# Optimization experiments

Measured on AMD Instinct MI355X. Metric: run time of the kernel, lower is better.

The kernel has to match this reference:

```python
import jax, jax.numpy as jnp
import numpy as np
from jax import lax

RATIOS = (0.5, 1.0, 2.0)
LEVEL_SCALES = (4, 8, 16, 32)
FEAT_STRIDE = (4, 8, 16, 32)
BASE_SIZE = 16.0
NMS_THRESH = 0.7
PRE_NMS = 2000
POST_NMS = 300
MIN_SIZE = 16.0
SCALE = 1.0


def _anchor_base(scale):
    # chainercv-style anchor base: (y1, x1, y2, x2) centered at base_size/2
    py = px = BASE_SIZE / 2.0
    ab = np.zeros((len(RATIOS), 4), np.float32)
    for i, r in enumerate(RATIOS):
        h = BASE_SIZE * scale * np.sqrt(r)
        w = BASE_SIZE * scale * np.sqrt(1.0 / r)
        ab[i] = [py - h / 2.0, px - w / 2.0, py + h / 2.0, px + w / 2.0]
    return ab


def _shifted_anchors(level, hh, ww):
    ab = _anchor_base(LEVEL_SCALES[level])
    stride = FEAT_STRIDE[level]
    sy = np.arange(0, hh * stride, stride)
    sx = np.arange(0, ww * stride, stride)
    sx, sy = np.meshgrid(sx, sy)
    shift = np.stack((sy.ravel(), sx.ravel(), sy.ravel(), sx.ravel()), axis=1)
    A, K = ab.shape[0], shift.shape[0]
    anchor = ab.reshape(1, A, 4) + shift.reshape(1, K, 4).transpose(1, 0, 2)
    return anchor.reshape(K * A, 4).astype(np.float32)


def _conv(x, w, b, pad):
    y = lax.conv_general_dilated(x, w, (1, 1), [(pad, pad), (pad, pad)],
                                 dimension_numbers=("NCHW", "OIHW", "NCHW"))
    return y + b[None, :, None, None]


def _iou_matrix(b):
    y1, x1, y2, x2 = b[:, 0], b[:, 1], b[:, 2], b[:, 3]
    area = (y2 - y1) * (x2 - x1)
    iy = jnp.maximum(0.0, jnp.minimum(y2[:, None], y2[None, :]) - jnp.maximum(y1[:, None], y1[None, :]))
    ix = jnp.maximum(0.0, jnp.minimum(x2[:, None], x2[None, :]) - jnp.maximum(x1[:, None], x1[None, :]))
    inter = iy * ix
    return inter / (area[:, None] + area[None, :] - inter + 1e-10)


def _greedy_nms(boxes, keep0):
    # boxes are sorted by descending score; sequential greedy suppression
    n = boxes.shape[0]
    iou = _iou_matrix(boxes)  # [PRE_NMS, PRE_NMS]
    idx = jnp.arange(n)

    def body(i, keep):
        sup = jnp.where(keep[i], iou[i] > NMS_THRESH, False) & (idx > i)
        return keep & ~sup

    return lax.fori_loop(0, n, body, keep0)


def _proposal_single(loc, fg, anchors, img_h, img_w):
    # loc2bbox decode
    ah = anchors[:, 2] - anchors[:, 0]
    aw = anchors[:, 3] - anchors[:, 1]
    acy = anchors[:, 0] + 0.5 * ah
    acx = anchors[:, 1] + 0.5 * aw
    cy = loc[:, 0] * ah + acy
    cx = loc[:, 1] * aw + acx
    h = jnp.exp(loc[:, 2]) * ah
    w = jnp.exp(loc[:, 3]) * aw
    boxes = jnp.stack([cy - 0.5 * h, cx - 0.5 * w, cy + 0.5 * h, cx + 0.5 * w], axis=-1)
    hi = jnp.array([img_h, img_w, img_h, img_w], dtype=boxes.dtype)
    boxes = jnp.clip(boxes, 0.0, hi)
    hs = boxes[:, 2] - boxes[:, 0]
    ws = boxes[:, 3] - boxes[:, 1]
    valid = (hs >= MIN_SIZE * SCALE) & (ws >= MIN_SIZE * SCALE)
    sc = jnp.where(valid, fg, -jnp.inf)
    top_sc, top_idx = lax.top_k(sc, PRE_NMS)
    tb = boxes[top_idx]
    keep = _greedy_nms(tb, top_sc > -jnp.inf)
    order = jnp.argsort(jnp.where(keep, 0, 1), stable=True)[:POST_NMS]
    roi = jnp.where(keep[order][:, None], tb[order], 0.0)
    return roi  # [POST_NMS, 4] zero-padded


def _head(fm, conv1_w, conv1_b, score_w, score_b, loc_w, loc_b):
    B, _, hh, ww = fm.shape
    h = jax.nn.relu(_conv(fm, conv1_w, conv1_b, 1))
    locs = _conv(h, loc_w, loc_b, 0).transpose(0, 2, 3, 1).reshape(B, -1, 4)
    scores = _conv(h, score_w, score_b, 0).transpose(0, 2, 3, 1)  # [B,hh,ww,6]
    fg = jax.nn.softmax(scores.reshape(B, hh, ww, 3, 2), axis=-1)[..., 1].reshape(B, -1)
    return locs, scores.reshape(B, -1, 2), fg


def setup_inputs() -> dict:
    key = jax.random.key(0)
    ks = jax.random.split(key, 10)
    d = {
        "fm0": jax.random.normal(ks[0], (2, 512, 200, 200), jnp.float32),
        "fm1": jax.random.normal(ks[1], (2, 512, 100, 100), jnp.float32),
        "fm2": jax.random.normal(ks[2], (2, 512, 50, 50), jnp.float32),
        "fm3": jax.random.normal(ks[3], (2, 512, 25, 25), jnp.float32),
        "conv1_w": jax.random.normal(ks[4], (512, 512, 3, 3), jnp.float32) * 0.01,
        "conv1_b": jnp.zeros((512,), jnp.float32),
        "score_w": jax.random.normal(ks[5], (6, 512, 1, 1), jnp.float32) * 0.01,
        "score_b": jnp.zeros((6,), jnp.float32),
        "loc_w": jax.random.normal(ks[6], (12, 512, 1, 1), jnp.float32) * 0.01,
        "loc_b": jnp.zeros((12,), jnp.float32),
        "img_h": 800,
        "img_w": 800,
    }
    return d


def reference(fm0, fm1, fm2, fm3, conv1_w, conv1_b, score_w, score_b, loc_w, loc_b, img_h, img_w):
    fms = [fm0, fm1, fm2, fm3]
    B = fm0.shape[0]
    all_locs, all_scores, all_fg, anchors_np = [], [], [], []
    for i, fm in enumerate(fms):
        hh, ww = fm.shape[2], fm.shape[3]
        anchors_np.append(_shifted_anchors(i, hh, ww))
        locs, scores, fg = _head(fm, conv1_w, conv1_b, score_w, score_b, loc_w, loc_b)
        all_locs.append(locs)
        all_scores.append(scores)
        all_fg.append(fg)
    rpn_locs = jnp.concatenate(all_locs, axis=1)      # [B, A, 4]
    rpn_scores = jnp.concatenate(all_scores, axis=1)  # [B, A, 2]
    rpn_fg = jnp.concatenate(all_fg, axis=1)          # [B, A]
    anchors = jnp.asarray(np.concatenate(anchors_np, axis=0))
    # proposal layer operates on detached numpy data in the original
    rois = jax.vmap(lambda l, s: _proposal_single(l, s, anchors, img_h, img_w))(
        lax.stop_gradient(rpn_locs), lax.stop_gradient(rpn_fg))
    rois = rois.reshape(-1, 4)
    roi_indices = jnp.repeat(jnp.arange(B, dtype=jnp.int32), POST_NMS)
    return rpn_locs, rpn_scores, rois, roi_indices, anchors
```

## Files before the change

### kernel.cpp

```cpp
#include <hip/hip_runtime.h>
#include <math.h>

#define NA 159375
static constexpr size_t OFF_LOCS   = 0;
static constexpr size_t OFF_SCORES = 1275000;
static constexpr size_t OFF_ROIS   = 1912500;
static constexpr size_t OFF_RI     = 1914900;
static constexpr size_t OFF_ANCH   = 1915500;
#define MONO_NEGINF 0x007FFFFFu

__global__ void k_wT(const float* __restrict__ w, float* __restrict__ wT) {
  int idx = blockIdx.x * 256 + threadIdx.x;
  if (idx >= 512 * 512 * 9) return;
  int oc = idx & 511;
  int row = idx >> 9;
  int ic = row / 9, tap = row - ic * 9;
  wT[idx] = w[((size_t)oc * 512 + ic) * 9 + tap];
}

__global__
__attribute__((amdgpu_flat_work_group_size(512, 512), amdgpu_waves_per_eu(2, 4)))
void k_conv(
    const float* __restrict__ fm0, const float* __restrict__ fm1,
    const float* __restrict__ fm2, const float* __restrict__ fm3,
    const float* __restrict__ wT,
    const float* __restrict__ cb, const float* __restrict__ locw,
    const float* __restrict__ locb, const float* __restrict__ scow,
    const float* __restrict__ scob, float* __restrict__ out) {
  const int tb_ = blockIdx.x;
  const int b = blockIdx.y;
  int H, locbase, nt, tile;
  const float* fmb;
  if (tb_ < 625)      { H = 200; locbase = 0;     nt = 25; tile = tb_;       fmb = fm0; }
  else if (tb_ < 794) { H = 100; locbase = 40000; nt = 13; tile = tb_ - 625; fmb = fm1; }
  else if (tb_ < 843) { H = 50;  locbase = 50000; nt = 7;  tile = tb_ - 794; fmb = fm2; }
  else                { H = 25;  locbase = 52500; nt = 4;  tile = tb_ - 843; fmb = fm3; }
  const int W = H;
  const int ty_t = tile / nt, tx_t = tile - ty_t * nt;
  const int x0 = tx_t * 8, y0 = ty_t * 8;
  fmb += (size_t)b * 512 * H * W;

  const int tid = threadIdx.x;
  const int pxg = tid & 15, ocg = tid >> 4;
  const int ty = pxg >> 1, tx0 = (pxg & 1) * 4;

  __shared__ alignas(16) union LDS {
    struct { float w[2 * 9 * 512]; float in[2][10][12]; } m;
    struct { float h[64 * 132]; float w1[18 * 128]; } e;
  } lds;

  float acc[4][16];
#pragma unroll
  for (int q = 0; q < 4; q++)
#pragma unroll
    for (int i = 0; i < 16; i++) acc[q][i] = 0.f;

#pragma unroll 1
  for (int ic0 = 0; ic0 < 512; ic0 += 2) {
    __syncthreads();
    const float2* wsrc = reinterpret_cast<const float2*>(wT + (size_t)ic0 * 9 * 512);
    float2* wdst = reinterpret_cast<float2*>(lds.m.w);
#pragma unroll
    for (int r = 0; r < 9; r++) wdst[r * 512 + tid] = wsrc[r * 512 + tid];
    if (tid < 200) {
      int ic = tid / 100, rem = tid % 100, rr = rem / 10, cc = rem % 10;
      int yy = y0 - 1 + rr, xx = x0 - 1 + cc;
      float v = 0.f;
      if (yy >= 0 && yy < H && xx >= 0 && xx < W)
        v = fmb[((size_t)(ic0 + ic) * H + yy) * W + xx];
      lds.m.in[ic][rr][cc] = v;
    }
    __syncthreads();
#pragma unroll
    for (int ic = 0; ic < 2; ic++) {
#pragma unroll
      for (int ky = 0; ky < 3; ky++) {
        const float* rowp = &lds.m.in[ic][ty + ky][tx0];
        float4 rlo = *reinterpret_cast<const float4*>(rowp);
        float2 rhi = *reinterpret_cast<const float2*>(rowp + 4);
        float r[6] = {rlo.x, rlo.y, rlo.z, rlo.w, rhi.x, rhi.y};
#pragma unroll
        for (int kx = 0; kx < 3; kx++) {
          const float4* wp = reinterpret_cast<const float4*>(
              &lds.m.w[(ic * 9 + ky * 3 + kx) * 512 + ocg * 16]);
#pragma unroll
          for (int v4 = 0; v4 < 4; v4++) {
            float4 wv = wp[v4];
#pragma unroll
            for (int q = 0; q < 4; q++) {
              float iv = r[q + kx];
              acc[q][v4 * 4 + 0] = fmaf(iv, wv.x, acc[q][v4 * 4 + 0]);
              acc[q][v4 * 4 + 1] = fmaf(iv, wv.y, acc[q][v4 * 4 + 1]);
              acc[q][v4 * 4 + 2] = fmaf(iv, wv.z, acc[q][v4 * 4 + 2]);
              acc[q][v4 * 4 + 3] = fmaf(iv, wv.w, acc[q][v4 * 4 + 3]);
            }
          }
        }
      }
    }
  }
#pragma unroll
  for (int i = 0; i < 16; i++) {
    float bb = cb[ocg * 16 + i];
#pragma unroll
    for (int q = 0; q < 4; q++) acc[q][i] = fmaxf(__fadd_rn(acc[q][i], bb), 0.f);
  }

  float part[3] = {0.f, 0.f, 0.f};
#pragma unroll 1
  for (int c = 0; c < 4; c++) {
    __syncthreads();
    for (int idx = tid; idx < 18 * 128; idx += 512) {
      int ch = idx >> 7, j = idx & 127;
      lds.e.w1[idx] = (ch < 12) ? locw[ch * 512 + c * 128 + j]
                                : scow[(ch - 12) * 512 + c * 128 + j];
    }
    if ((ocg >> 3) == c) {
      int ocl = (ocg & 7) * 16;
#pragma unroll
      for (int q = 0; q < 4; q++)
#pragma unroll
        for (int i = 0; i < 16; i++)
          lds.e.h[(pxg * 4 + q) * 132 + ocl + i] = acc[q][i];
    }
    __syncthreads();
#pragma unroll
    for (int pp = 0; pp < 3; pp++) {
      int pair = tid + pp * 512;
      if (pair < 1152) {
        int px = pair & 63, ch = pair >> 6;
        const float4* hp = reinterpret_cast<const float4*>(&lds.e.h[px * 132]);
        const float4* wp = reinterpret_cast<const float4*>(&lds.e.w1[ch * 128]);
        float s = part[pp];
#pragma unroll
        for (int j = 0; j < 32; j++) {
          float4 h4 = hp[j], w4 = wp[j];
          s = fmaf(h4.x, w4.x, fmaf(h4.y, w4.y, fmaf(h4.z, w4.z, fmaf(h4.w, w4.w, s))));
        }
        part[pp] = s;
      }
    }
  }
#pragma unroll
  for (int pp = 0; pp < 3; pp++) {
    int pair = tid + pp * 512;
    if (pair < 1152) {
      int px = pair & 63, ch = pair >> 6;
      int y = y0 + (px >> 3), x = x0 + (px & 7);
      if (y < H && x < W) {
        int k = locbase + y * W + x;
        if (ch < 12) {
          int a = ch >> 2, d = ch & 3;
          int n = 3 * k + a;
          out[OFF_LOCS + ((size_t)b * NA + n) * 4 + d] = __fadd_rn(part[pp], locb[ch]);
        } else {
          int s = ch - 12, a = s >> 1, si = s & 1;
          int n = 3 * k + a;
          out[OFF_SCORES + ((size_t)b * NA + n) * 2 + si] = __fadd_rn(part[pp], scob[s]);
        }
      }
    }
  }
}

__global__ void k_anchors(float* __restrict__ out) {
  int n = blockIdx.x * 256 + threadIdx.x;
  if (n >= NA) return;
  int a = n % 3, k = n / 3;
  int base, Wl, stride, scale;
  if (k < 40000)      { base = 0;     Wl = 200; stride = 4;  scale = 4; }
  else if (k < 50000) { base = 40000; Wl = 100; stride = 8;  scale = 8; }
  else if (k < 52500) { base = 50000; Wl = 50;  stride = 16; scale = 16; }
  else                { base = 52500; Wl = 25;  stride = 32; scale = 32; }
  int kk = k - base;
  int ky = kk / Wl, kx = kk - ky * Wl;
  double r = (a == 0) ? 0.5 : ((a == 1) ? 1.0 : 2.0);
  double sc = (double)scale;
  double h = (16.0 * sc) * sqrt(r);
  double w = (16.0 * sc) * sqrt(1.0 / r);
  float ab0 = (float)(8.0 - h / 2.0), ab1 = (float)(8.0 - w / 2.0);
  float ab2 = (float)(8.0 + h / 2.0), ab3 = (float)(8.0 + w / 2.0);
  double sy = (double)(ky * stride), sx = (double)(kx * stride);
  out[OFF_ANCH + (size_t)n * 4 + 0] = (float)((double)ab0 + sy);
  out[OFF_ANCH + (size_t)n * 4 + 1] = (float)((double)ab1 + sx);
  out[OFF_ANCH + (size_t)n * 4 + 2] = (float)((double)ab2 + sy);
  out[OFF_ANCH + (size_t)n * 4 + 3] = (float)((double)ab3 + sx);
}

__global__ void k_zero(unsigned* hhi, unsigned* hlo, unsigned* misc) {
  int i = blockIdx.x * 256 + threadIdx.x;
  if (i < 2 * 65536) { hhi[i] = 0u; hlo[i] = 0u; }
  if (i < 64) misc[i] = 0u;
}

__global__ void k_decode(const float* __restrict__ out, float* __restrict__ boxes,
                         unsigned* __restrict__ keys, const int* __restrict__ ihp,
                         const int* __restrict__ iwp) {
  int n = blockIdx.x * 256 + threadIdx.x;
  int b = blockIdx.y;
  if (n >= NA) return;
  const float* an = out + OFF_ANCH + (size_t)n * 4;
  float a0 = an[0], a1 = an[1], a2 = an[2], a3 = an[3];
  const float* lc = out + OFF_LOCS + ((size_t)b * NA + n) * 4;
  float l0 = lc[0], l1 = lc[1], l2 = lc[2], l3 = lc[3];
  const float* sp = out + OFF_SCORES + ((size_t)b * NA + n) * 2;
  float s0 = sp[0], s1 = sp[1];
  float m = fmaxf(s0, s1);
  float e0 = expf(__fsub_rn(s0, m)), e1 = expf(__fsub_rn(s1, m));
  float fg = __fdiv_rn(e1, __fadd_rn(e0, e1));
  float ah = __fsub_rn(a2, a0), aw = __fsub_rn(a3, a1);
  float acy = __fadd_rn(a0, __fmul_rn(0.5f, ah));
  float acx = __fadd_rn(a1, __fmul_rn(0.5f, aw));
  float cy = __fadd_rn(__fmul_rn(l0, ah), acy);
  float cx = __fadd_rn(__fmul_rn(l1, aw), acx);
  float hh = __fmul_rn(expf(l2), ah), ww = __fmul_rn(expf(l3), aw);
  float y1 = __fsub_rn(cy, __fmul_rn(0.5f, hh));
  float x1 = __fsub_rn(cx, __fmul_rn(0.5f, ww));
  float y2 = __fadd_rn(cy, __fmul_rn(0.5f, hh));
  float x2 = __fadd_rn(cx, __fmul_rn(0.5f, ww));
  float fh = (float)ihp[0], fw = (float)iwp[0];
  y1 = fminf(fmaxf(y1, 0.f), fh); x1 = fminf(fmaxf(x1, 0.f), fw);
  y2 = fminf(fmaxf(y2, 0.f), fh); x2 = fminf(fmaxf(x2, 0.f), fw);
  float hs = __fsub_rn(y2, y1), wsz = __fsub_rn(x2, x1);
  bool valid = (hs >= 16.f) && (wsz >= 16.f);
  float scv = valid ? fg : -INFINITY;
  size_t bi = (size_t)b * NA + n;
  boxes[bi * 4 + 0] = y1; boxes[bi * 4 + 1] = x1;
  boxes[bi * 4 + 2] = y2; boxes[bi * 4 + 3] = x2;
  unsigned u = __float_as_uint(scv);
  keys[bi] = (u & 0x80000000u) ? ~u : (u | 0x80000000u);
}

__global__ void k_hist_hi(const unsigned* __restrict__ keys, unsigned* __restrict__ hhi) {
  int n = blockIdx.x * 256 + threadIdx.x;
  int b = blockIdx.y;
  if (n >= NA) return;
  unsigned k = keys[(size_t)b * NA + n];
  atomicAdd(&hhi[b * 65536 + (k >> 16)], 1u);
}

__global__ void k_hist_lo(const unsigned* __restrict__ keys, const unsigned* __restrict__ misc,
                          unsigned* __restrict__ hlo) {
  int n = blockIdx.x * 256 + threadIdx.x;
  int b = blockIdx.y;
  if (n >= NA) return;
  unsigned bhi = misc[b * 32 + 2];
  unsigned k = keys[(size_t)b * NA + n];
  if ((k >> 16) == bhi) atomicAdd(&hlo[b * 65536 + (k & 0xFFFFu)], 1u);
}

__global__ __launch_bounds__(1024) void k_scan(const unsigned* __restrict__ hist,
                                               unsigned* __restrict__ misc, int mode) {
  int b = blockIdx.x;
  const unsigned* h = hist + (size_t)b * 65536;
  unsigned* mc = misc + b * 32;
  __shared__ unsigned part[1024];
  int t = threadIdx.x;
  unsigned target = (mode == 0) ? 2000u : mc[3];
  unsigned s = 0;
  for (int i = 0; i < 64; i++) s += h[t * 64 + i];
  part[t] = s;
  __syncthreads();
  if (t == 0) {
    unsigned cum = 0; int seg = 0;
    for (int u = 1023; u >= 0; --u) {
      if (cum + part[u] >= target) { seg = u; break; }
      cum += part[u];
    }
    unsigned c2 = cum; int bin = seg * 64;
    for (int v = seg * 64 + 63; v >= seg * 64; --v) {
      if (c2 + h[v] >= target) { bin = v; break; }
      c2 += h[v];
    }
    if (mode == 0) { mc[2] = (unsigned)bin; mc[3] = target - c2; }
    else {
      unsigned T = (mc[2] << 16) | (unsigned)bin;
      unsigned cnt_gt = (2000u - mc[3]) + c2;
      mc[4] = T; mc[5] = cnt_gt; mc[6] = 2000u - cnt_gt;
    }
  }
}

__global__ void k_collect(const unsigned* __restrict__ keys, unsigned* __restrict__ misc,
                          unsigned long long* __restrict__ sel, unsigned* __restrict__ ties) {
  int n = blockIdx.x * 256 + threadIdx.x;
  int b = blockIdx.y;
  if (n >= NA) return;
  unsigned T = misc[b * 32 + 4];
  unsigned k = keys[(size_t)b * NA + n];
  if (k > T) {
    unsigned p = atomicAdd(&misc[b * 32 + 0], 1u);
    if (p < 2048) sel[(size_t)b * 2048 + p] = ((unsigned long long)k << 32) | (unsigned)(~n);
  } else if (k == T) {
    unsigned p = atomicAdd(&misc[b * 32 + 1], 1u);
    if (p < 8192) ties[(size_t)b * 8192 + p] = (unsigned)n;
  }
}

__global__ __launch_bounds__(1024) void k_final(
    const unsigned long long* __restrict__ sel, const unsigned* __restrict__ ties,
    const unsigned* __restrict__ misc, const float* __restrict__ boxes,
    float* __restrict__ tb, unsigned long long* __restrict__ keepw) {
  int b = blockIdx.x, t = threadIdx.x;
  __shared__ unsigned tie_s[8192];
  __shared__ unsigned long long arr[2048];
  __shared__ unsigned long long kw[32];
  unsigned cnt_gt = misc[b * 32 + 5];
  unsigned cnt_eq = misc[b * 32 + 1]; if (cnt_eq > 8192u) cnt_eq = 8192u;
  unsigned T = misc[b * 32 + 4];
  unsigned msort = 64;
  while (msort < cnt_eq) msort <<= 1;
  for (int i = t; i < 8192; i += 1024)
    tie_s[i] = (i < (int)cnt_eq) ? ties[(size_t)b * 8192 + i] : 0xFFFFFFFFu;
  __syncthreads();
  for (unsigned kk = 2; kk <= msort; kk <<= 1)
    for (unsigned j = kk >> 1; j > 0; j >>= 1) {
      for (int i = t; i < (int)msort; i += 1024) {
        int l = i ^ (int)j;
        if (l > i) {
          unsigned a = tie_s[i], c = tie_s[l];
          bool up = ((i & kk) == 0);
          if ((a > c) == up) { tie_s[i] = c; tie_s[l] = a; }
        }
      }
      __syncthreads();
    }
  for (int i = t; i < 2048; i += 1024) {
    unsigned long long v = 0ull;
    if (i < (int)cnt_gt) v = sel[(size_t)b * 2048 + i];
    else if (i < 2000) {
      unsigned n = tie_s[i - cnt_gt];
      v = ((unsigned long long)T << 32) | (unsigned)(~n);
    }
    arr[i] = v;
  }
  __syncthreads();
  for (unsigned kk = 2; kk <= 2048; kk <<= 1)
    for (unsigned j = kk >> 1; j > 0; j >>= 1) {
      for (int i = t; i < 2048; i += 1024) {
        int l = i ^ (int)j;
        if (l > i) {
          unsigned long long a = arr[i], c = arr[l];
          bool dir = ((i & kk) != 0);
          if ((a > c) == dir) { arr[i] = c; arr[l] = a; }
        }
      }
      __syncthreads();
    }
  if (t < 32) kw[t] = 0ull;
  __syncthreads();
  for (int j = t; j < 2000; j += 1024) {
    unsigned long long v = arr[j];
    unsigned n = ~(unsigned)(v & 0xFFFFFFFFull);
    unsigned key = (unsigned)(v >> 32);
    const float* bp = boxes + ((size_t)b * NA + n) * 4;
    float* tp = tb + ((size_t)b * 2000 + j) * 4;
    tp[0] = bp[0]; tp[1] = bp[1]; tp[2] = bp[2]; tp[3] = bp[3];
    if (key > MONO_NEGINF) atomicOr(&kw[j >> 6], 1ull << (j & 63));
  }
  __syncthreads();
  if (t < 32) keepw[b * 32 + t] = kw[t];
}

__device__ __forceinline__ int swz(int i) { return i + (i >> 8); }
__global__ __launch_bounds__(256) void k_iou(const float* __restrict__ tb,
                                             unsigned long long* __restrict__ mask) {
  int b = blockIdx.y;
  __shared__ float bx[8032];
  const float* tbb = tb + (size_t)b * 2000 * 4;
  for (int i = threadIdx.x; i < 8000; i += 256) bx[swz(i)] = tbb[i];
  __syncthreads();
  int il = threadIdx.x >> 5, w = threadIdx.x & 31;
  int i = blockIdx.x * 8 + il;
  int ib = i * 4, ip = ib + (ib >> 8);
  float y1 = bx[ip], x1 = bx[ip + 1], y2 = bx[ip + 2], x2 = bx[ip + 3];
  float ai = __fmul_rn(__fsub_rn(y2, y1), __fsub_rn(x2, x1));
  unsigned long long m = 0ull;
  int j0 = w * 64;
  for (int l = 0; l < 64; l++) {
    int j = j0 + l;
    if (j < 2000 && j > i) {
      int jb = j * 4, jp = jb + (jb >> 8);
      float yy1 = bx[jp], xx1 = bx[jp + 1], yy2 = bx[jp + 2], xx2 = bx[jp + 3];
      float aj = __fmul_rn(__fsub_rn(yy2, yy1), __fsub_rn(xx2, xx1));
      float iy = fmaxf(0.f, __fsub_rn(fminf(y2, yy2), fmaxf(y1, yy1)));
      float ix = fmaxf(0.f, __fsub_rn(fminf(x2, xx2), fmaxf(x1, xx1)));
      float inter = __fmul_rn(iy, ix);
      float den = __fadd_rn(__fsub_rn(__fadd_rn(ai, aj), inter), 1e-10f);
      if (__fdiv_rn(inter, den) > 0.7f) m |= (1ull << l);
    }
  }
  mask[((size_t)b * 2000 + i) * 32 + w] = m;
}

__device__ __forceinline__ unsigned long long shfl64(unsigned long long v, int src) {
  int lo = __shfl((int)(v & 0xFFFFFFFFull), src, 64);
  int hi = __shfl((int)(v >> 32), src, 64);
  return ((unsigned long long)(unsigned)hi << 32) | (unsigned)lo;
}
__global__ __launch_bounds__(64) void k_nms(const unsigned long long* __restrict__ mask,
                                            unsigned long long* __restrict__ keepw) {
  int b = blockIdx.x, lane = threadIdx.x;
  __shared__ unsigned long long rows[64][33];
  unsigned long long k = (lane < 32) ? keepw[b * 32 + lane] : 0ull;
  const unsigned long long* mb = mask + (size_t)b * 2000 * 32;
  for (int c = 0; c < 32; c++) {
    __syncthreads();
    for (int it = 0; it < 32; it++) {
      int idx = it * 64 + lane;
      int r = idx >> 5, w = idx & 31;
      int gi = c * 64 + r;
      rows[r][w] = (gi < 2000) ? mb[(size_t)gi * 32 + w] : 0ull;
    }
    __syncthreads();
    for (int il = 0; il < 64; il++) {
      int i = c * 64 + il;
      if (i >= 2000) break;
      unsigned long long kv = shfl64(k, i >> 6);
      if ((kv >> (i & 63)) & 1ull) {
        if (lane < 32) k &= ~rows[il][lane];
      }
    }
  }
  if (lane < 32) keepw[b * 32 + lane] = k;
}

__global__ __launch_bounds__(1024) void k_rois(const unsigned long long* __restrict__ keepw,
                                               const float* __restrict__ tb,
                                               float* __restrict__ out) {
  int b = blockIdx.x, t = threadIdx.x;
  __shared__ unsigned long long kws[32];
  __shared__ unsigned pre[33];
  if (t < 32) kws[t] = keepw[b * 32 + t];
  __syncthreads();
  if (t == 0) {
    unsigned c = 0;
    for (int w = 0; w < 32; w++) { pre[w] = c; c += __popcll(kws[w]); }
    pre[32] = c;
  }
  __syncthreads();
  unsigned total = pre[32];
  for (int j = t; j < 2000; j += 1024) {
    unsigned long long kv = kws[j >> 6];
    if ((kv >> (j & 63)) & 1ull) {
      unsigned rank = pre[j >> 6] + (unsigned)__popcll(kv & ((1ull << (j & 63)) - 1ull));
      if (rank < 300) {
        const float* tp = tb + ((size_t)b * 2000 + j) * 4;
        float* op = out + OFF_ROIS + ((size_t)b * 300 + rank) * 4;
        op[0] = tp[0]; op[1] = tp[1]; op[2] = tp[2]; op[3] = tp[3];
      }
    }
  }
  for (int r = t; r < 300; r += 1024) {
    if ((unsigned)r >= total) {
      float* op = out + OFF_ROIS + ((size_t)b * 300 + r) * 4;
      op[0] = 0.f; op[1] = 0.f; op[2] = 0.f; op[3] = 0.f;
    }
    out[OFF_RI + b * 300 + r] = (float)b;
  }
}

extern "C" void kernel_launch(void* const* d_in, const int* in_sizes, int n_in,
                              void* d_out, int out_size, void* d_ws, size_t ws_size,
                              hipStream_t stream) {
  const float* fm0 = (const float*)d_in[0];
  const float* fm1 = (const float*)d_in[1];
  const float* fm2 = (const float*)d_in[2];
  const float* fm3 = (const float*)d_in[3];
  const float* cw  = (const float*)d_in[4];
  const float* cb  = (const float*)d_in[5];
  const float* scw = (const float*)d_in[6];
  const float* scb = (const float*)d_in[7];
  const float* lw  = (const float*)d_in[8];
  const float* lb  = (const float*)d_in[9];
  const int* ih = (const int*)d_in[10];
  const int* iw = (const int*)d_in[11];
  float* out = (float*)d_out;
  char* wsb = (char*)d_ws;

  auto al = [](size_t x) { return (x + 511) & ~(size_t)511; };
  size_t off = 0;
  float* wT = (float*)(wsb + off);                 off = al(off + (size_t)512 * 512 * 9 * 4);
  float* boxes = (float*)(wsb + off);              off = al(off + (size_t)2 * NA * 4 * 4);
  unsigned* keys = (unsigned*)(wsb + off);         off = al(off + (size_t)2 * NA * 4);
  unsigned* hhi = (unsigned*)(wsb + off);          off = al(off + (size_t)2 * 65536 * 4);
  unsigned* hlo = (unsigned*)(wsb + off);          off = al(off + (size_t)2 * 65536 * 4);
  unsigned* misc = (unsigned*)(wsb + off);         off = al(off + 64 * 4);
  unsigned long long* sel = (unsigned long long*)(wsb + off);  off = al(off + (size_t)2 * 2048 * 8);
  unsigned* ties = (unsigned*)(wsb + off);         off = al(off + (size_t)2 * 8192 * 4);
  float* tb = (float*)(wsb + off);                 off = al(off + (size_t)2 * 2000 * 4 * 4);
  unsigned long long* mask = (unsigned long long*)(wsb + off); off = al(off + (size_t)2 * 2000 * 32 * 8);
  unsigned long long* keep = (unsigned long long*)(wsb + off); off = al(off + (size_t)2 * 32 * 8);
  (void)ws_size; (void)in_sizes; (void)n_in; (void)out_size;

  k_wT<<<dim3((512 * 512 * 9 + 255) / 256), dim3(256), 0, stream>>>(cw, wT);

  k_conv<<<dim3(859, 2), dim3(512), 0, stream>>>(fm0, fm1, fm2, fm3, wT, cb,
                                                 lw, lb, scw, scb, out);
  k_anchors<<<dim3(623), dim3(256), 0, stream>>>(out);
  k_zero<<<dim3(512), dim3(256), 0, stream>>>(hhi, hlo, misc);
  k_decode<<<dim3(623, 2), dim3(256), 0, stream>>>(out, boxes, keys, ih, iw);
  k_hist_hi<<<dim3(623, 2), dim3(256), 0, stream>>>(keys, hhi);
  k_scan<<<dim3(2), dim3(1024), 0, stream>>>(hhi, misc, 0);
  k_hist_lo<<<dim3(623, 2), dim3(256), 0, stream>>>(keys, misc, hlo);
  k_scan<<<dim3(2), dim3(1024), 0, stream>>>(hlo, misc, 1);
  k_collect<<<dim3(623, 2), dim3(256), 0, stream>>>(keys, misc, sel, ties);
  k_final<<<dim3(2), dim3(1024), 0, stream>>>(sel, ties, misc, boxes, tb, keep);
  k_iou<<<dim3(250, 2), dim3(256), 0, stream>>>(tb, mask);
  k_nms<<<dim3(2), dim3(64), 0, stream>>>(mask, keep);
  k_rois<<<dim3(2), dim3(1024), 0, stream>>>(keep, tb, out);
}
```

Measured before the change: 8.144 ms.

## Enlarge conv tile to 16x8 pixels with 8 outputs per thread

The 3x3 conv kernel now gives each block a 16-row by 8-column pixel tile, and each thread computes one full row of 8 pixels for 16 output channels. This halves the number of blocks, so each LDS weight tile loaded per input-channel pair is reused across twice as many pixels. It also precomputes the staging offsets and rotates the LDS read order in the 1x1 head dot product to avoid bank conflicts. In exchange the accumulators grow to 128 registers per thread, which lowers occupancy, and fewer blocks (452 per batch) may underfill the GPU.

```diff
diff --git a/kernel.cpp b/kernel.cpp
--- a/kernel.cpp
+++ b/kernel.cpp
@@ -29,56 +29,64 @@
     const float* __restrict__ scob, float* __restrict__ out) {
   const int tb_ = blockIdx.x;
   const int b = blockIdx.y;
-  int H, locbase, nt, tile;
+  int H, locbase, ncol, tile;
   const float* fmb;
-  if (tb_ < 625)      { H = 200; locbase = 0;     nt = 25; tile = tb_;       fmb = fm0; }
-  else if (tb_ < 794) { H = 100; locbase = 40000; nt = 13; tile = tb_ - 625; fmb = fm1; }
-  else if (tb_ < 843) { H = 50;  locbase = 50000; nt = 7;  tile = tb_ - 794; fmb = fm2; }
-  else                { H = 25;  locbase = 52500; nt = 4;  tile = tb_ - 843; fmb = fm3; }
+  if (tb_ < 325)      { H = 200; locbase = 0;     ncol = 25; tile = tb_;       fmb = fm0; }
+  else if (tb_ < 416) { H = 100; locbase = 40000; ncol = 13; tile = tb_ - 325; fmb = fm1; }
+  else if (tb_ < 444) { H = 50;  locbase = 50000; ncol = 7;  tile = tb_ - 416; fmb = fm2; }
+  else                { H = 25;  locbase = 52500; ncol = 4;  tile = tb_ - 444; fmb = fm3; }
   const int W = H;
-  const int ty_t = tile / nt, tx_t = tile - ty_t * nt;
-  const int x0 = tx_t * 8, y0 = ty_t * 8;
+  const int ty_t = tile / ncol, tx_t = tile - ty_t * ncol;
+  const int y0 = ty_t * 16, x0 = tx_t * 8;
   fmb += (size_t)b * 512 * H * W;
 
   const int tid = threadIdx.x;
-  const int pxg = tid & 15, ocg = tid >> 4;
-  const int ty = pxg >> 1, tx0 = (pxg & 1) * 4;
+  const int pxg = tid & 15;
+  const int ocg = tid >> 4;
 
   __shared__ alignas(16) union LDS {
-    struct { float w[2 * 9 * 512]; float in[2][10][12]; } m;
-    struct { float h[64 * 132]; float w1[18 * 128]; } e;
+    struct { float w[9216]; float in[2][18][12]; } m;
+    struct { float h[128 * 132]; float w1[2304]; } e;
   } lds;
 
-  float acc[4][16];
-#pragma unroll
-  for (int q = 0; q < 4; q++)
+  float acc[8][16];
+#pragma unroll
+  for (int q = 0; q < 8; q++)
 #pragma unroll
     for (int i = 0; i < 16; i++) acc[q][i] = 0.f;
 
+  const bool stg = (tid < 360);
+  int sic = 0, srr = 0, scc = 0; bool sok = false; size_t soff = 0;
+  if (stg) {
+    sic = tid / 180; int rem = tid % 180; srr = rem / 10; scc = rem % 10;
+    int yy = y0 - 1 + srr, xx = x0 - 1 + scc;
+    sok = (yy >= 0 && yy < H && xx >= 0 && xx < W);
+    if (sok) soff = ((size_t)sic * H + yy) * W + xx;
+  }
+  const size_t icstep = (size_t)2 * H * W;
+
 #pragma unroll 1
-  for (int ic0 = 0; ic0 < 512; ic0 += 2) {
+  for (int t = 0; t < 256; ++t) {
     __syncthreads();
-    const float2* wsrc = reinterpret_cast<const float2*>(wT + (size_t)ic0 * 9 * 512);
+    const float2* wsrc = reinterpret_cast<const float2*>(wT + (size_t)t * 9216);
     float2* wdst = reinterpret_cast<float2*>(lds.m.w);
 #pragma unroll
     for (int r = 0; r < 9; r++) wdst[r * 512 + tid] = wsrc[r * 512 + tid];
-    if (tid < 200) {
-      int ic = tid / 100, rem = tid % 100, rr = rem / 10, cc = rem % 10;
-      int yy = y0 - 1 + rr, xx = x0 - 1 + cc;
+    if (stg) {
       float v = 0.f;
-      if (yy >= 0 && yy < H && xx >= 0 && xx < W)
-        v = fmb[((size_t)(ic0 + ic) * H + yy) * W + xx];
-      lds.m.in[ic][rr][cc] = v;
+      if (sok) v = fmb[(size_t)t * icstep + soff];
+      lds.m.in[sic][srr][scc] = v;
     }
     __syncthreads();
 #pragma unroll
     for (int ic = 0; ic < 2; ic++) {
 #pragma unroll
       for (int ky = 0; ky < 3; ky++) {
-        const float* rowp = &lds.m.in[ic][ty + ky][tx0];
-        float4 rlo = *reinterpret_cast<const float4*>(rowp);
-        float2 rhi = *reinterpret_cast<const float2*>(rowp + 4);
-        float r[6] = {rlo.x, rlo.y, rlo.z, rlo.w, rhi.x, rhi.y};
+        const float* rowp = &lds.m.in[ic][pxg + ky][0];
+        float4 ra = *reinterpret_cast<const float4*>(rowp);
+        float4 rb = *reinterpret_cast<const float4*>(rowp + 4);
+        float2 rc = *reinterpret_cast<const float2*>(rowp + 8);
+        float r[10] = {ra.x, ra.y, ra.z, ra.w, rb.x, rb.y, rb.z, rb.w, rc.x, rc.y};
 #pragma unroll
         for (int kx = 0; kx < 3; kx++) {
           const float4* wp = reinterpret_cast<const float4*>(
@@ -87,7 +95,7 @@
           for (int v4 = 0; v4 < 4; v4++) {
             float4 wv = wp[v4];
 #pragma unroll
-            for (int q = 0; q < 4; q++) {
+            for (int q = 0; q < 8; q++) {
               float iv = r[q + kx];
               acc[q][v4 * 4 + 0] = fmaf(iv, wv.x, acc[q][v4 * 4 + 0]);
               acc[q][v4 * 4 + 1] = fmaf(iv, wv.y, acc[q][v4 * 4 + 1]);
@@ -103,14 +111,14 @@
   for (int i = 0; i < 16; i++) {
     float bb = cb[ocg * 16 + i];
 #pragma unroll
-    for (int q = 0; q < 4; q++) acc[q][i] = fmaxf(__fadd_rn(acc[q][i], bb), 0.f);
-  }
-
-  float part[3] = {0.f, 0.f, 0.f};
+    for (int q = 0; q < 8; q++) acc[q][i] = fmaxf(__fadd_rn(acc[q][i], bb), 0.f);
+  }
+
+  float part[5] = {0.f, 0.f, 0.f, 0.f, 0.f};
 #pragma unroll 1
   for (int c = 0; c < 4; c++) {
     __syncthreads();
-    for (int idx = tid; idx < 18 * 128; idx += 512) {
+    for (int idx = tid; idx < 2304; idx += 512) {
       int ch = idx >> 7, j = idx & 127;
       lds.e.w1[idx] = (ch < 12) ? locw[ch * 512 + c * 128 + j]
                                 : scow[(ch - 12) * 512 + c * 128 + j];
@@ -118,34 +126,37 @@
     if ((ocg >> 3) == c) {
       int ocl = (ocg & 7) * 16;
 #pragma unroll
-      for (int q = 0; q < 4; q++)
-#pragma unroll
-        for (int i = 0; i < 16; i++)
-          lds.e.h[(pxg * 4 + q) * 132 + ocl + i] = acc[q][i];
+      for (int q = 0; q < 8; q++)
+#pragma unroll
+        for (int i4 = 0; i4 < 4; i4++)
+          *reinterpret_cast<float4*>(&lds.e.h[(pxg * 8 + q) * 132 + ocl + i4 * 4]) =
+              *reinterpret_cast<const float4*>(&acc[q][i4 * 4]);
     }
     __syncthreads();
-#pragma unroll
-    for (int pp = 0; pp < 3; pp++) {
+#pragma unroll 1
+    for (int pp = 0; pp < 5; pp++) {
       int pair = tid + pp * 512;
-      if (pair < 1152) {
-        int px = pair & 63, ch = pair >> 6;
-        const float4* hp = reinterpret_cast<const float4*>(&lds.e.h[px * 132]);
-        const float4* wp = reinterpret_cast<const float4*>(&lds.e.w1[ch * 128]);
+      if (pair < 2304) {
+        int px = pair & 127, ch = pair >> 7;
+        const float* hb = &lds.e.h[px * 132];
+        const float* w1b = &lds.e.w1[ch * 128];
         float s = part[pp];
 #pragma unroll
         for (int j = 0; j < 32; j++) {
-          float4 h4 = hp[j], w4 = wp[j];
+          int slot = (j + px) & 31;
+          float4 h4 = *reinterpret_cast<const float4*>(hb + slot * 4);
+          float4 w4 = *reinterpret_cast<const float4*>(w1b + slot * 4);
           s = fmaf(h4.x, w4.x, fmaf(h4.y, w4.y, fmaf(h4.z, w4.z, fmaf(h4.w, w4.w, s))));
         }
         part[pp] = s;
       }
     }
   }
-#pragma unroll
-  for (int pp = 0; pp < 3; pp++) {
+#pragma unroll 1
+  for (int pp = 0; pp < 5; pp++) {
     int pair = tid + pp * 512;
-    if (pair < 1152) {
-      int px = pair & 63, ch = pair >> 6;
+    if (pair < 2304) {
+      int px = pair & 127, ch = pair >> 7;
       int y = y0 + (px >> 3), x = x0 + (px & 7);
       if (y < H && x < W) {
         int k = locbase + y * W + x;
@@ -495,7 +506,7 @@
 
   k_wT<<<dim3((512 * 512 * 9 + 255) / 256), dim3(256), 0, stream>>>(cw, wT);
 
-  k_conv<<<dim3(859, 2), dim3(512), 0, stream>>>(fm0, fm1, fm2, fm3, wT, cb,
+  k_conv<<<dim3(452, 2), dim3(512), 0, stream>>>(fm0, fm1, fm2, fm3, wT, cb,
                                                  lw, lb, scw, scb, out);
   k_anchors<<<dim3(623), dim3(256), 0, stream>>>(out);
   k_zero<<<dim3(512), dim3(256), 0, stream>>>(hhi, hlo, misc);
```

Result: no change. 8.112 ms (-0.4%).
